# Optimization experiments

Measured on AMD Instinct MI355X. Metric: run time of the kernel, lower is better.

Reference implementation:

```python
import jax, jax.numpy as jnp
import numpy as np


def setup_inputs() -> dict:
    key = jax.random.key(0)
    ks = jax.random.split(key, 8)
    B, N, A, H = 2, 2048, 256, 8
    KD = A // H  # key_dim per head = 32
    VD = A // H  # value_dim per head = 32
    return {
        "q_data": jax.random.normal(ks[0], (B, N, A), dtype=jnp.float32),
        "bias": jax.random.normal(ks[1], (B, N), dtype=jnp.float32),
        "nonbatched_bias": jax.random.normal(ks[2], (H, N, N), dtype=jnp.float32),
        "query_w": jax.random.normal(ks[3], (A, H, KD), dtype=jnp.float32) * 0.05,
        "query_b": jax.random.normal(ks[4], (1, H, KD), dtype=jnp.float32) * 0.05,
        "key_w": jax.random.normal(ks[5], (A, H, KD), dtype=jnp.float32) * 0.05,
        "value_w": jax.random.normal(ks[6], (A, H, VD), dtype=jnp.float32) * 0.05,
        "gating_w": jax.random.normal(ks[7], (A, H, VD), dtype=jnp.float32) * 0.05,
    }


def reference(q_data, bias, nonbatched_bias, query_w, query_b, key_w, value_w, gating_w):
    # q_data: [b, n, a]; bias: [b, n_k]; nonbatched_bias: [h, n_q, n_k]
    key_dim = query_w.shape[-1]
    scale = key_dim ** (-0.5)
    # projections (fused QKV in the original kernel)
    q = (jnp.einsum("bqa,ahc->bqhc", q_data, query_w) + query_b) * scale  # [b,q,h,c]
    k = jnp.einsum("bka,ahc->bkhc", q_data, key_w)                        # [b,k,h,c]
    v = jnp.einsum("bka,ahv->bkhv", q_data, value_w)                      # [b,k,h,v]
    # attention logits + batched bias (over keys) + shared nonbatched bias
    logits = jnp.einsum("bqhc,bkhc->bhqk", q, k)
    logits = logits + bias[:, None, None, :] + nonbatched_bias[None]
    weights = jax.nn.softmax(logits, axis=-1)                             # [b,h,q,k]
    weighted = jnp.einsum("bhqk,bkhv->bqhv", weights, v)                  # [b,q,h,v]
    # sigmoid gating branch fused after value projection
    gate = jax.nn.sigmoid(jnp.einsum("bqa,ahv->bqhv", q_data, gating_w))
    return weighted * gate                                                # [b,q,h,v]
```

## Files before the change

### kernel.cpp

```cpp
#include <hip/hip_runtime.h>
#include <stdint.h>

#define NTOK 2048
#define SCALE 0.17677669529663687f
#define SM_SHIFT 24.0f

typedef short s16x8 __attribute__((ext_vector_type(8)));
typedef unsigned short u16x8 __attribute__((ext_vector_type(8)));
typedef float f32x4 __attribute__((ext_vector_type(4)));

__device__ __forceinline__ unsigned short f2bf(float f) {
  unsigned int u = __builtin_bit_cast(unsigned int, f);
  u += 0x7fffu + ((u >> 16) & 1u);
  return (unsigned short)(u >> 16);
}

__global__ __launch_bounds__(256) void prep_weights_k(
    const float* __restrict__ qw, const float* __restrict__ kw,
    const float* __restrict__ vw, const float* __restrict__ gw,
    unsigned short* __restrict__ Wt) {
  __shared__ float tile[64][68];
  const int p = blockIdx.z;
  const int a0 = blockIdx.x * 64;
  const int n0 = blockIdx.y * 64;
  const float* src = (p == 0) ? qw : (p == 1) ? kw : (p == 2) ? vw : gw;
  const int tx = threadIdx.x & 15;
  const int ty = threadIdx.x >> 4;
#pragma unroll
  for (int kk = 0; kk < 4; kk++) {
    int ar = ty + kk * 16;
    float4 v = *reinterpret_cast<const float4*>(src + (a0 + ar) * 256 + n0 + tx * 4);
    tile[ar][tx * 4 + 0] = v.x; tile[ar][tx * 4 + 1] = v.y;
    tile[ar][tx * 4 + 2] = v.z; tile[ar][tx * 4 + 3] = v.w;
  }
  __syncthreads();
  unsigned short* dst = Wt + p * 65536;
#pragma unroll
  for (int kk = 0; kk < 4; kk++) {
    int nr = ty + kk * 16;
    ushort4 o;
    o.x = f2bf(tile[tx * 4 + 0][nr]);
    o.y = f2bf(tile[tx * 4 + 1][nr]);
    o.z = f2bf(tile[tx * 4 + 2][nr]);
    o.w = f2bf(tile[tx * 4 + 3][nr]);
    *reinterpret_cast<ushort4*>(dst + (n0 + nr) * 256 + a0 + tx * 4) = o;
  }
}

__global__ __launch_bounds__(256) void proj_k(
    const float* __restrict__ x, const unsigned short* __restrict__ Wt,
    const float* __restrict__ query_b,
    unsigned short* __restrict__ Qg, unsigned short* __restrict__ Kg,
    unsigned short* __restrict__ Vt, float* __restrict__ gate) {
  const int w = threadIdx.x >> 6;
  const int lane = threadIdx.x & 63;
  const int l15 = lane & 15;
  const int quad = lane >> 4;
  const int p = blockIdx.y >> 1;
  const int half = blockIdx.y & 1;
  const int rbase = blockIdx.x * 128 + w * 32;
  const unsigned short* wp = Wt + p * 65536;

  f32x4 acc[2][8];
#pragma unroll
  for (int rt = 0; rt < 2; rt++)
#pragma unroll
    for (int ct = 0; ct < 8; ct++) acc[rt][ct] = (f32x4){0.f, 0.f, 0.f, 0.f};

  for (int ks = 0; ks < 8; ks++) {
    const int kb = ks * 32;
    s16x8 af[2];
#pragma unroll
    for (int rt = 0; rt < 2; rt++) {
      const float* xr = x + (rbase + rt * 16 + l15) * 256 + kb + quad * 8;
      float4 f0 = *reinterpret_cast<const float4*>(xr);
      float4 f1 = *reinterpret_cast<const float4*>(xr + 4);
      u16x8 t;
      t[0] = f2bf(f0.x); t[1] = f2bf(f0.y); t[2] = f2bf(f0.z); t[3] = f2bf(f0.w);
      t[4] = f2bf(f1.x); t[5] = f2bf(f1.y); t[6] = f2bf(f1.z); t[7] = f2bf(f1.w);
      af[rt] = __builtin_bit_cast(s16x8, t);
    }
#pragma unroll
    for (int ct = 0; ct < 8; ct++) {
      uint4 bv = *reinterpret_cast<const uint4*>(
          wp + (half * 128 + ct * 16 + l15) * 256 + kb + quad * 8);
      s16x8 bfr = __builtin_bit_cast(s16x8, bv);
#pragma unroll
      for (int rt = 0; rt < 2; rt++)
        acc[rt][ct] = __builtin_amdgcn_mfma_f32_16x16x32_bf16(af[rt], bfr, acc[rt][ct], 0, 0, 0);
    }
  }

#pragma unroll
  for (int ct = 0; ct < 8; ct++) {
    const int cgl = half * 128 + ct * 16 + l15;
    const int h = cgl >> 5, c = cgl & 31;
#pragma unroll
    for (int rt = 0; rt < 2; rt++) {
      const int n0r = rbase + rt * 16 + quad * 4;
      const int bidx = n0r >> 11;
      const int nl0 = n0r & 2047;
      if (p == 0) {
        const float qb = query_b[cgl];
#pragma unroll
        for (int i = 0; i < 4; i++) {
          float v = (acc[rt][ct][i] + qb) * SCALE;
          Qg[(size_t)((bidx * 8 + h) * 2048 + nl0 + i) * 32 + c] = f2bf(v);
        }
      } else if (p == 1) {
#pragma unroll
        for (int i = 0; i < 4; i++)
          Kg[(size_t)((bidx * 8 + h) * 2048 + nl0 + i) * 32 + c] = f2bf(acc[rt][ct][i]);
      } else if (p == 2) {
        ushort4 o;
        o.x = f2bf(acc[rt][ct][0]); o.y = f2bf(acc[rt][ct][1]);
        o.z = f2bf(acc[rt][ct][2]); o.w = f2bf(acc[rt][ct][3]);
        *reinterpret_cast<ushort4*>(Vt + (size_t)((bidx * 8 + h) * 32 + c) * 2048 + nl0) = o;
      } else {
#pragma unroll
        for (int i = 0; i < 4; i++) {
          float s = 1.f / (1.f + __expf(-acc[rt][ct][i]));
          gate[(size_t)(bidx * 2048 + nl0 + i) * 256 + cgl] = s;
        }
      }
    }
  }
}

#define PST 72
__global__ __launch_bounds__(128, 4) void attn_k(
    const unsigned short* __restrict__ Qg, const unsigned short* __restrict__ Kg,
    const unsigned short* __restrict__ Vt, const float* __restrict__ bias,
    const float* __restrict__ nb,
    float* __restrict__ po, float* __restrict__ pl) {
  __shared__ unsigned short Ps[2 * 16 * PST];
  const int w = threadIdx.x >> 6;
  const int lane = threadIdx.x & 63;
  const int l15 = lane & 15;
  const int quad = lane >> 4;
  const int h = blockIdx.y;
  const int b = blockIdx.z >> 1;
  const int sp = blockIdx.z & 1;
  const int bh = b * 8 + h;
  const int qbase = blockIdx.x * 32 + w * 16;
  const int kt0 = sp * 16;
  const unsigned short* Qp = Qg + (size_t)bh * 2048 * 32;
  const unsigned short* Kp = Kg + (size_t)bh * 2048 * 32;
  const unsigned short* Vp = Vt + (size_t)bh * 32 * 2048;
  const float* nbp = nb + (size_t)h * 2048 * 2048;
  const float* biasp = bias + b * 2048;
  unsigned short* Pw = Ps + w * 16 * PST;

  s16x8 aq = __builtin_bit_cast(s16x8, *reinterpret_cast<const uint4*>(
      Qp + (size_t)(qbase + l15) * 32 + quad * 8));
  const int qr0 = qbase + quad * 4;

  float lst[4];
  f32x4 o[2];
#pragma unroll
  for (int i = 0; i < 4; i++) lst[i] = 0.f;
#pragma unroll
  for (int vt = 0; vt < 2; vt++) o[vt] = (f32x4){0.f, 0.f, 0.f, 0.f};

  float nbuf[16];
  float bb[4];
#pragma unroll
  for (int ct = 0; ct < 4; ct++) {
    bb[ct] = biasp[kt0 * 64 + ct * 16 + l15];
#pragma unroll
    for (int i = 0; i < 4; i++)
      nbuf[ct * 4 + i] = nbp[(size_t)(qr0 + i) * 2048 + kt0 * 64 + ct * 16 + l15];
  }

#pragma unroll 2
  for (int kt = kt0; kt < kt0 + 16; kt++) {
    const int kb = kt * 64;

    s16x8 bk[4];
#pragma unroll
    for (int ct = 0; ct < 4; ct++)
      bk[ct] = __builtin_bit_cast(s16x8, *reinterpret_cast<const uint4*>(
          Kp + (size_t)(kb + ct * 16 + l15) * 32 + quad * 8));

    s16x8 vbf[2][2];
#pragma unroll
    for (int kc = 0; kc < 2; kc++)
#pragma unroll
      for (int vt = 0; vt < 2; vt++)
        vbf[kc][vt] = __builtin_bit_cast(s16x8, *reinterpret_cast<const uint4*>(
            Vp + (size_t)(vt * 16 + l15) * 2048 + kb + kc * 32 + quad * 8));

    f32x4 s[4];
#pragma unroll
    for (int ct = 0; ct < 4; ct++)
      s[ct] = __builtin_amdgcn_mfma_f32_16x16x32_bf16(
          aq, bk[ct], (f32x4){0.f, 0.f, 0.f, 0.f}, 0, 0, 0);

#pragma unroll
    for (int ct = 0; ct < 4; ct++)
#pragma unroll
      for (int i = 0; i < 4; i++) s[ct][i] += bb[ct] + nbuf[ct * 4 + i];

    if (kt < kt0 + 15) {
      const int kb2 = kb + 64;
      __builtin_amdgcn_sched_barrier(0);
#pragma unroll
      for (int ct = 0; ct < 4; ct++) {
        bb[ct] = biasp[kb2 + ct * 16 + l15];
#pragma unroll
        for (int i = 0; i < 4; i++)
          nbuf[ct * 4 + i] = nbp[(size_t)(qr0 + i) * 2048 + kb2 + ct * 16 + l15];
      }
      __builtin_amdgcn_sched_barrier(0);
    }

#pragma unroll
    for (int i = 0; i < 4; i++) {
      float sum = 0.f;
#pragma unroll
      for (int ct = 0; ct < 4; ct++) {
        float pv = __expf(s[ct][i] - SM_SHIFT);
        Pw[(quad * 4 + i) * PST + ct * 16 + l15] = f2bf(pv);
        sum += pv;
      }
      lst[i] += sum;
    }

#pragma unroll
    for (int kc = 0; kc < 2; kc++) {
      s16x8 ap = __builtin_bit_cast(s16x8, *reinterpret_cast<const uint4*>(
          &Pw[l15 * PST + kc * 32 + quad * 8]));
#pragma unroll
      for (int vt = 0; vt < 2; vt++)
        o[vt] = __builtin_amdgcn_mfma_f32_16x16x32_bf16(ap, vbf[kc][vt], o[vt], 0, 0, 0);
    }
  }

  const size_t pbase = (size_t)(sp * 16 + bh) * 2048;
#pragma unroll
  for (int vt = 0; vt < 2; vt++)
#pragma unroll
    for (int i = 0; i < 4; i++)
      po[(pbase + qr0 + i) * 32 + vt * 16 + l15] = o[vt][i];
#pragma unroll
  for (int i = 0; i < 4; i++) {
    lst[i] += __shfl_xor(lst[i], 1);
    lst[i] += __shfl_xor(lst[i], 2);
    lst[i] += __shfl_xor(lst[i], 4);
    lst[i] += __shfl_xor(lst[i], 8);
  }
  if (l15 == 0) {
#pragma unroll
    for (int i = 0; i < 4; i++) pl[pbase + qr0 + i] = lst[i];
  }
}

__global__ __launch_bounds__(256) void combine_k(
    const float* __restrict__ po, const float* __restrict__ pl,
    const float* __restrict__ gate, float* __restrict__ out) {
  const int bq = blockIdx.x;
  const int b = bq >> 11, q = bq & 2047;
  const int h = threadIdx.x >> 5, v = threadIdx.x & 31;
  const int bh = b * 8 + h;
  const size_t i0 = (size_t)(0 * 16 + bh) * 2048 + q;
  const size_t i1 = (size_t)(1 * 16 + bh) * 2048 + q;
  const float l = pl[i0] + pl[i1];
  const float ov = po[i0 * 32 + v] + po[i1 * 32 + v];
  const size_t oidx = (size_t)(b * 2048 + q) * 256 + h * 32 + v;
  out[oidx] = (ov / l) * gate[oidx];
}

extern "C" void kernel_launch(void* const* d_in, const int* in_sizes, int n_in,
                              void* d_out, int out_size, void* d_ws, size_t ws_size,
                              hipStream_t stream) {
  const float* q_data = (const float*)d_in[0];
  const float* bias = (const float*)d_in[1];
  const float* nbb = (const float*)d_in[2];
  const float* qw = (const float*)d_in[3];
  const float* qb = (const float*)d_in[4];
  const float* kw = (const float*)d_in[5];
  const float* vw = (const float*)d_in[6];
  const float* gw = (const float*)d_in[7];
  float* out = (float*)d_out;

  char* ws = (char*)d_ws;
  unsigned short* Wt = (unsigned short*)(ws + 0);
  unsigned short* Qg = (unsigned short*)(ws + 524288);
  unsigned short* Kg = (unsigned short*)(ws + 2621440);
  unsigned short* Vt = (unsigned short*)(ws + 4718592);
  float* gate = (float*)(ws + 6815744);
  float* po = (float*)(ws + 11010048);
  float* pl = (float*)(ws + 19398656);

  prep_weights_k<<<dim3(4, 4, 4), 256, 0, stream>>>(qw, kw, vw, gw, Wt);
  proj_k<<<dim3(32, 8), 256, 0, stream>>>(q_data, Wt, qb, Qg, Kg, Vt, gate);
  attn_k<<<dim3(64, 8, 4), 128, 0, stream>>>(Qg, Kg, Vt, bias, nbb, po, pl);
  combine_k<<<dim3(4096), 256, 0, stream>>>(po, pl, gate, out);
}
```

Measured before the change: 293.6 us.

## Share nonbatched bias tile across batches via async global-to-LDS double buffer

```diff
diff --git a/kernel.cpp b/kernel.cpp
--- a/kernel.cpp
+++ b/kernel.cpp
@@ -13,6 +13,12 @@
   unsigned int u = __builtin_bit_cast(unsigned int, f);
   u += 0x7fffu + ((u >> 16) & 1u);
   return (unsigned short)(u >> 16);
+}
+
+__device__ __forceinline__ void gld_lds16(const float* g, float* l) {
+  __builtin_amdgcn_global_load_lds(
+      (const __attribute__((address_space(1))) unsigned int*)g,
+      (__attribute__((address_space(3))) unsigned int*)l, 16, 0, 0);
 }
 
 __global__ __launch_bounds__(256) void prep_weights_k(
@@ -128,33 +134,54 @@
 }
 
 #define PST 72
-__global__ __launch_bounds__(128, 4) void attn_k(
+__global__ __launch_bounds__(256, 4) void attn_k(
     const unsigned short* __restrict__ Qg, const unsigned short* __restrict__ Kg,
     const unsigned short* __restrict__ Vt, const float* __restrict__ bias,
     const float* __restrict__ nb,
     float* __restrict__ po, float* __restrict__ pl) {
-  __shared__ unsigned short Ps[2 * 16 * PST];
+  __shared__ float NbS[2][32 * 64];
+  __shared__ unsigned short Ps[4 * 16 * PST];
   const int w = threadIdx.x >> 6;
   const int lane = threadIdx.x & 63;
   const int l15 = lane & 15;
   const int quad = lane >> 4;
+  const int qsub = w >> 1;
+  const int b = w & 1;
   const int h = blockIdx.y;
-  const int b = blockIdx.z >> 1;
-  const int sp = blockIdx.z & 1;
+  const int sp = blockIdx.z;
   const int bh = b * 8 + h;
-  const int qbase = blockIdx.x * 32 + w * 16;
+  const int qtile = blockIdx.x * 32;
+  const int qbase = qtile + qsub * 16;
   const int kt0 = sp * 16;
   const unsigned short* Qp = Qg + (size_t)bh * 2048 * 32;
   const unsigned short* Kp = Kg + (size_t)bh * 2048 * 32;
   const unsigned short* Vp = Vt + (size_t)bh * 32 * 2048;
-  const float* nbp = nb + (size_t)h * 2048 * 2048;
   const float* biasp = bias + b * 2048;
   unsigned short* Pw = Ps + w * 16 * PST;
+
+  const float* nbl[2];
+  {
+    const float* nbt = nb + (size_t)h * 2048 * 2048 + (size_t)qtile * 2048;
+#pragma unroll
+    for (int j = 0; j < 2; j++) {
+      const int r = w * 8 + j * 4 + (lane >> 4);
+      const int cblk = (lane & 15) ^ (r & 7);
+      nbl[j] = nbt + (size_t)r * 2048 + cblk * 4;
+    }
+  }
 
   s16x8 aq = __builtin_bit_cast(s16x8, *reinterpret_cast<const uint4*>(
       Qp + (size_t)(qbase + l15) * 32 + quad * 8));
   const int qr0 = qbase + quad * 4;
 
+  int nbrow[4], nbkey[4];
+#pragma unroll
+  for (int i = 0; i < 4; i++) {
+    const int rl = qsub * 16 + quad * 4 + i;
+    nbrow[i] = rl * 64;
+    nbkey[i] = rl & 7;
+  }
+
   float lst[4];
   f32x4 o[2];
 #pragma unroll
@@ -162,19 +189,19 @@
 #pragma unroll
   for (int vt = 0; vt < 2; vt++) o[vt] = (f32x4){0.f, 0.f, 0.f, 0.f};
 
-  float nbuf[16];
   float bb[4];
 #pragma unroll
-  for (int ct = 0; ct < 4; ct++) {
-    bb[ct] = biasp[kt0 * 64 + ct * 16 + l15];
-#pragma unroll
-    for (int i = 0; i < 4; i++)
-      nbuf[ct * 4 + i] = nbp[(size_t)(qr0 + i) * 2048 + kt0 * 64 + ct * 16 + l15];
-  }
+  for (int ct = 0; ct < 4; ct++) bb[ct] = biasp[kt0 * 64 + ct * 16 + l15];
+
+#pragma unroll
+  for (int j = 0; j < 2; j++)
+    gld_lds16(nbl[j] + kt0 * 64, &NbS[0][(w * 8 + j * 4) * 64]);
+  __syncthreads();
 
 #pragma unroll 2
   for (int kt = kt0; kt < kt0 + 16; kt++) {
     const int kb = kt * 64;
+    const int cur = kt & 1, nxt = cur ^ 1;
 
     s16x8 bk[4];
 #pragma unroll
@@ -190,28 +217,30 @@
         vbf[kc][vt] = __builtin_bit_cast(s16x8, *reinterpret_cast<const uint4*>(
             Vp + (size_t)(vt * 16 + l15) * 2048 + kb + kc * 32 + quad * 8));
 
+    if (kt < kt0 + 15) {
+#pragma unroll
+      for (int j = 0; j < 2; j++)
+        gld_lds16(nbl[j] + (kb + 64), &NbS[nxt][(w * 8 + j * 4) * 64]);
+    }
+
     f32x4 s[4];
 #pragma unroll
+    for (int ct = 0; ct < 4; ct++) {
+#pragma unroll
+      for (int i = 0; i < 4; i++) {
+        const int slot = ((ct * 4 + (l15 >> 2)) ^ nbkey[i]) * 4 + (l15 & 3);
+        s[ct][i] = bb[ct] + NbS[cur][nbrow[i] + slot];
+      }
+    }
+
+#pragma unroll
     for (int ct = 0; ct < 4; ct++)
-      s[ct] = __builtin_amdgcn_mfma_f32_16x16x32_bf16(
-          aq, bk[ct], (f32x4){0.f, 0.f, 0.f, 0.f}, 0, 0, 0);
-
-#pragma unroll
-    for (int ct = 0; ct < 4; ct++)
-#pragma unroll
-      for (int i = 0; i < 4; i++) s[ct][i] += bb[ct] + nbuf[ct * 4 + i];
+      s[ct] = __builtin_amdgcn_mfma_f32_16x16x32_bf16(aq, bk[ct], s[ct], 0, 0, 0);
 
     if (kt < kt0 + 15) {
       const int kb2 = kb + 64;
-      __builtin_amdgcn_sched_barrier(0);
-#pragma unroll
-      for (int ct = 0; ct < 4; ct++) {
-        bb[ct] = biasp[kb2 + ct * 16 + l15];
-#pragma unroll
-        for (int i = 0; i < 4; i++)
-          nbuf[ct * 4 + i] = nbp[(size_t)(qr0 + i) * 2048 + kb2 + ct * 16 + l15];
-      }
-      __builtin_amdgcn_sched_barrier(0);
+#pragma unroll
+      for (int ct = 0; ct < 4; ct++) bb[ct] = biasp[kb2 + ct * 16 + l15];
     }
 
 #pragma unroll
@@ -234,6 +263,8 @@
       for (int vt = 0; vt < 2; vt++)
         o[vt] = __builtin_amdgcn_mfma_f32_16x16x32_bf16(ap, vbf[kc][vt], o[vt], 0, 0, 0);
     }
+
+    __syncthreads();
   }
 
   const size_t pbase = (size_t)(sp * 16 + bh) * 2048;
@@ -294,6 +325,6 @@
 
   prep_weights_k<<<dim3(4, 4, 4), 256, 0, stream>>>(qw, kw, vw, gw, Wt);
   proj_k<<<dim3(32, 8), 256, 0, stream>>>(q_data, Wt, qb, Qg, Kg, Vt, gate);
-  attn_k<<<dim3(64, 8, 4), 128, 0, stream>>>(Qg, Kg, Vt, bias, nbb, po, pl);
+  attn_k<<<dim3(64, 8, 2), 256, 0, stream>>>(Qg, Kg, Vt, bias, nbb, po, pl);
   combine_k<<<dim3(4096), 256, 0, stream>>>(po, pl, gate, out);
 }
```

New measurement: 253.6 us. -13.6%, faster.
